# Kernel tuning notes

Hardware: AMD Instinct MI355X
Metric: run time of the kernel (lower is better)

## Reference

```python
import jax, jax.numpy as jnp
import numpy as np

EPS = 1e-5

def bn_eval(x, p):
    # p: [4, C] = gamma, beta, running_mean, running_var; channel-last broadcast
    g, b, m, v = p[0], p[1], p[2], p[3]
    return (x - m) * (g / jnp.sqrt(v + EPS)) + b

def _bn_params(k, c):
    k1, k2, k3, k4 = jax.random.split(k, 4)
    gamma = jax.random.uniform(k1, (c,)) + 0.5
    beta = jax.random.normal(k2, (c,)) * 0.1
    mean = jax.random.normal(k3, (c,)) * 0.1
    var = jax.random.uniform(k4, (c,)) + 0.5
    return jnp.stack([gamma, beta, mean, var])

def _lin(k, fan_in, fan_out):
    bound = 1.0 / np.sqrt(fan_in)
    kw, kb = jax.random.split(k)
    w = jax.random.uniform(kw, (fan_in, fan_out), minval=-bound, maxval=bound)
    b = jax.random.uniform(kb, (fan_out,), minval=-bound, maxval=bound)
    return w, b

def setup_inputs() -> dict:
    key = jax.random.key(0)
    B, N, S, C, G = 2, 4096, 16, 256, 8
    ks = jax.random.split(key, 20)
    feats = jax.random.normal(ks[0], (B, N, C), dtype=jnp.float32)
    coords = jax.random.normal(ks[1], (B, N, 3), dtype=jnp.float32)
    index = jax.random.randint(ks[2], (B, N, S), 0, N, dtype=jnp.int32)
    wq, bq = _lin(ks[3], C, C); bnq = _bn_params(ks[4], C)
    wk, bk = _lin(ks[5], C, C); bnk = _bn_params(ks[6], C)
    wv, bv = _lin(ks[7], C, C)
    pm_w1, pm_b1 = _lin(ks[8], 3, C); pm_bn = _bn_params(ks[9], C)
    pm_w2, pm_b2 = _lin(ks[10], C, C)
    pb_w1, pb_b1 = _lin(ks[11], 3, C); pb_bn = _bn_params(ks[12], C)
    pb_w2, pb_b2 = _lin(ks[13], C, C)
    we_w1, we_b1 = _lin(ks[14], C, G); we_bn = _bn_params(ks[15], G)
    we_w2, we_b2 = _lin(ks[16], G, G)
    return dict(feats=feats, coords=coords, index=index,
                wq=wq, bq=bq, bnq=bnq, wk=wk, bk=bk, bnk=bnk, wv=wv, bv=bv,
                pm_w1=pm_w1, pm_b1=pm_b1, pm_bn=pm_bn, pm_w2=pm_w2, pm_b2=pm_b2,
                pb_w1=pb_w1, pb_b1=pb_b1, pb_bn=pb_bn, pb_w2=pb_w2, pb_b2=pb_b2,
                we_w1=we_w1, we_b1=we_b1, we_bn=we_bn, we_w2=we_w2, we_b2=we_b2)

def reference(feats, coords, index,
              wq, bq, bnq, wk, bk, bnk, wv, bv,
              pm_w1, pm_b1, pm_bn, pm_w2, pm_b2,
              pb_w1, pb_b1, pb_bn, pb_w2, pb_b2,
              we_w1, we_b1, we_bn, we_w2, we_b2):
    B, N, C = feats.shape
    S = index.shape[2]
    G = we_w1.shape[1]
    q = jax.nn.relu(bn_eval(feats @ wq + bq, bnq))                       # [B,N,C]
    k = jax.nn.relu(bn_eval(feats @ wk + bk, bnk))                       # [B,N,C]
    v = feats @ wv + bv                                                   # [B,N,C]
    idx = index.reshape(B, N * S)
    key_g = jnp.take_along_axis(k, idx[:, :, None], axis=1).reshape(B, N, S, C)
    val_g = jnp.take_along_axis(v, idx[:, :, None], axis=1).reshape(B, N, S, C)
    crd_g = jnp.take_along_axis(coords, idx[:, :, None], axis=1).reshape(B, N, S, 3)
    relation_qk = key_g - q[:, :, None, :]                                # [B,N,S,C]
    pos = coords[:, :, None, :] - crd_g                                   # [B,N,S,3]
    pem = jax.nn.relu(bn_eval(pos @ pm_w1 + pm_b1, pm_bn)) @ pm_w2 + pm_b2
    relation_qk = relation_qk * pem
    peb = jax.nn.relu(bn_eval(pos @ pb_w1 + pb_b1, pb_bn)) @ pb_w2 + pb_b2
    relation_qk = relation_qk + peb
    val_g = val_g + peb
    w = jax.nn.relu(bn_eval(relation_qk @ we_w1 + we_b1, we_bn)) @ we_w2 + we_b2  # [B,N,S,G]
    w = jax.nn.softmax(w, axis=2)                                         # softmax over neighbors
    val_g = val_g.reshape(B, N, S, G, C // G)
    out = jnp.einsum('bnsgi,bnsg->bngi', val_g, w).reshape(B, N, C)
    return out
```

## Files before the change

kernel.cpp:

```cpp
#include <hip/hip_runtime.h>
#include <hip/hip_bf16.h>


typedef __attribute__((ext_vector_type(8))) short bf16x8_t;
typedef __attribute__((ext_vector_type(4))) float f32x4_t;

#define BN_EPS 1e-5f
#define WSYNC() asm volatile("s_waitcnt lgkmcnt(0)" ::: "memory")

__device__ __forceinline__ float blo(unsigned int v) {
    union { unsigned int u; float f; } x; x.u = v << 16; return x.f;
}
__device__ __forceinline__ float bhi(unsigned int v) {
    union { unsigned int u; float f; } x; x.u = v & 0xffff0000u; return x.f;
}
__device__ __forceinline__ unsigned int fbits(float f) {
    union { float f; unsigned int u; } x; x.f = f; return x.u;
}
__device__ __forceinline__ unsigned short f2b(float f) {
    unsigned int u = fbits(f);
    return (unsigned short)((u + 0x7fffu + ((u >> 16) & 1u)) >> 16);
}
__device__ __forceinline__ unsigned int f2bpk(float a, float b) {
    union { __hip_bfloat162 h; unsigned int u; } x;
    x.h = __float22bfloat162_rn(make_float2(a, b));
    return x.u;
}
__device__ __forceinline__ unsigned int relpair(unsigned int kb, unsigned int qb,
                                                unsigned int pm_, unsigned int pb_) {
    float r0 = (blo(kb) - blo(qb)) * blo(pm_) + blo(pb_);
    float r1 = (bhi(kb) - bhi(qb)) * bhi(pm_) + bhi(pb_);
    return f2bpk(r0, r1);
}

__global__ __launch_bounds__(256) void k_prep(
    const float* __restrict__ wq, const float* __restrict__ wk,
    const float* __restrict__ wv, const float* __restrict__ pm2,
    const float* __restrict__ pb2,
    const float* __restrict__ pm_w1, const float* __restrict__ pm_b1,
    const float* __restrict__ pm_bn,
    const float* __restrict__ pb_w1, const float* __restrict__ pb_b1,
    const float* __restrict__ pb_bn,
    const float* __restrict__ we_w1,
    unsigned short* __restrict__ wsT, float* __restrict__ W4,
    unsigned short* __restrict__ we1TF)
{
    const int bid = blockIdx.x, t = threadIdx.x;
    if (bid < 160) {
        __shared__ unsigned short T[32][72];
        const int mat = bid >> 5;
        const int kk  = (bid >> 2) & 7;
        const int ntq = bid & 3;
        const float* s = (mat == 0) ? wq : (mat == 1) ? wk : (mat == 2) ? wv
                         : (mat == 3) ? pm2 : pb2;
        {
            int c = t & 63, r0 = t >> 6;
            for (int i = 0; i < 8; ++i) {
                int r = r0 + i * 4;
                T[r][c] = f2b(s[(kk * 32 + r) * 256 + ntq * 64 + c]);
            }
        }
        __syncthreads();
        {
            int seg = t >> 6, lane = t & 63;
            int col = seg * 16 + (lane & 15);
            int kr  = (lane >> 4) * 8;
            unsigned int v[8];
            #pragma unroll
            for (int j = 0; j < 8; ++j) v[j] = T[kr + j][col];
            uint4 o;
            o.x = v[0] | (v[1] << 16);
            o.y = v[2] | (v[3] << 16);
            o.z = v[4] | (v[5] << 16);
            o.w = v[6] | (v[7] << 16);
            *(uint4*)(wsT + mat * 65536 + (ntq * 4 + seg) * 4096 + kk * 512 + lane * 8) = o;
        }
    } else if (bid == 160) {
        int c = t;
        float s = pm_bn[c] / sqrtf(pm_bn[768 + c] + BN_EPS);
        float4 wm = make_float4(pm_w1[c] * s, pm_w1[256 + c] * s, pm_w1[512 + c] * s,
                                (pm_b1[c] - pm_bn[512 + c]) * s + pm_bn[256 + c]);
        s = pb_bn[c] / sqrtf(pb_bn[768 + c] + BN_EPS);
        float4 wb = make_float4(pb_w1[c] * s, pb_w1[256 + c] * s, pb_w1[512 + c] * s,
                                (pb_b1[c] - pb_bn[512 + c]) * s + pb_bn[256 + c]);
        ((float4*)W4)[c]       = wm;
        ((float4*)W4)[256 + c] = wb;
    } else {
        for (int j = 0; j < 8; ++j) {
            int e = t * 8 + j;
            int g = e >> 8, c = e & 255;
            we1TF[g * 256 + c] = f2b(we_w1[c * 8 + g]);
        }
    }
}

__global__ __launch_bounds__(256) void k_qkv(
    const float* __restrict__ feats,
    const unsigned short* __restrict__ wT,
    const float* __restrict__ bq, const float* __restrict__ bnq,
    const float* __restrict__ bk, const float* __restrict__ bnk,
    const float* __restrict__ bv,
    unsigned short* __restrict__ qkv)
{
    __shared__ unsigned short A[32][264];
    const int t    = threadIdx.x;
    const int widx = blockIdx.x >> 8;
    const int mb   = blockIdx.x & 255;

    for (int i = 0; i < 8; ++i) {
        int row = 4 * i + (t >> 6), col = (t & 63) * 4;
        float4 f = *(const float4*)(feats + (mb * 32 + row) * 256 + col);
        *(uint2*)&A[row][col] = make_uint2(f2bpk(f.x, f.y), f2bpk(f.z, f.w));
    }
    __syncthreads();

    const int lane = t & 63, w = t >> 6;
    const int ln15 = lane & 15, quad = lane >> 4;
    const int mt = w & 1, nh = w >> 1;

    bf16x8_t afr[8];
    #pragma unroll
    for (int kk = 0; kk < 8; ++kk)
        afr[kk] = *(const bf16x8_t*)&A[mt * 16 + ln15][kk * 32 + quad * 8];

    const unsigned short* W = wT + widx * 65536;
    const float* bias = (widx == 0) ? bq : (widx == 1) ? bk : bv;
    const float* bn   = (widx == 0) ? bnq : (widx == 1) ? bnk : nullptr;
    unsigned short* dst = qkv + (size_t)widx * 8192 * 256;

    f32x4_t acc[8];
    for (int j = 0; j < 8; ++j) acc[j] = (f32x4_t){0.f, 0.f, 0.f, 0.f};

    #pragma unroll
    for (int kk = 0; kk < 8; ++kk) {
        #pragma unroll
        for (int j = 0; j < 8; ++j) {
            int nt = nh * 8 + j;
            bf16x8_t bfr = *(const bf16x8_t*)(W + ((nt * 8 + kk) * 64 + lane) * 8);
            acc[j] = __builtin_amdgcn_mfma_f32_16x16x32_bf16(afr[kk], bfr, acc[j], 0, 0, 0);
        }
    }

    float bb[8], sc[8], mu[8], be[8];
    #pragma unroll
    for (int j = 0; j < 8; ++j) {
        int c = (nh * 8 + j) * 16 + ln15;
        bb[j] = bias[c];
        if (bn) {
            sc[j] = bn[c] / sqrtf(bn[768 + c] + BN_EPS);
            be[j] = bn[256 + c];
            mu[j] = bn[512 + c];
        }
    }
    __syncthreads();
    #pragma unroll
    for (int j = 0; j < 8; ++j) {
        int c = (nh * 8 + j) * 16 + ln15;
        float y[4];
        for (int r = 0; r < 4; ++r) {
            y[r] = acc[j][r] + bb[j];
            if (bn) y[r] = fmaxf((y[r] - mu[j]) * sc[j] + be[j], 0.f);
        }
        for (int r = 0; r < 4; r += 2) {
            unsigned int pk = f2bpk(y[r], y[r + 1]);
            A[mt * 16 + quad * 4 + r][c]     = (unsigned short)pk;
            A[mt * 16 + quad * 4 + r + 1][c] = (unsigned short)(pk >> 16);
        }
    }
    __syncthreads();
    {
        int row = t >> 3, cc = (t & 7) * 32;
        #pragma unroll
        for (int j = 0; j < 4; ++j) {
            uint4 v = *(const uint4*)&A[row][cc + 8 * j];
            *(uint4*)(dst + (mb * 32 + row) * 256 + cc + 8 * j) = v;
        }
    }
}

__global__ __launch_bounds__(512, 4) void k_main(
    const float* __restrict__ coords,
    const int*   __restrict__ index,
    const unsigned short* __restrict__ qm,
    const unsigned short* __restrict__ km,
    const unsigned short* __restrict__ vm,
    const unsigned short* __restrict__ pmw2F,
    const unsigned short* __restrict__ pbw2F,
    const float* __restrict__ W4,
    const unsigned short* __restrict__ we1TF,
    const float* __restrict__ pm_b2, const float* __restrict__ pb_b2,
    const float* __restrict__ we_b1, const float* __restrict__ we_bn,
    const float* __restrict__ we_w2, const float* __restrict__ we_b2,
    float* __restrict__ out)
{
    __shared__ unsigned short bufR[64][264];
    __shared__ unsigned short bufP[64][264];
    __shared__ float posA[64][4];
    __shared__ float usP[2][64][8];
    __shared__ float us_[64][8];
    __shared__ int   rowg_[64];
    __shared__ float we2s[8][8];
    __shared__ float web2[8], swe8[8], dwe8[8];

    const int t   = threadIdx.x;
    const int P0  = blockIdx.x * 4;
    const int bb_ = P0 >> 12;
    const int w = t >> 6, lane = t & 63;
    const int ln15 = lane & 15, quad = lane >> 4;
    const int p   = w >> 1, sub = w & 1;
    const int R0  = p * 16;
    const int Pg  = P0 + p;

    const int rg = (bb_ << 12) + index[Pg * 16 + ln15];
    uint4 kpre[4];
    #pragma unroll
    for (int kk = 0; kk < 4; ++kk)
        kpre[kk] = *(const uint4*)(km + rg * 256 + (sub * 4 + kk) * 32 + quad * 8);

    if (lane < 8) {
        int m  = w * 8 + lane;
        int Pr = P0 + (m >> 4);
        int rs = (bb_ << 12) + index[Pr * 16 + (m & 15)];
        rowg_[m]   = rs;
        posA[m][0] = coords[Pr * 3 + 0] - coords[rs * 3 + 0];
        posA[m][1] = coords[Pr * 3 + 1] - coords[rs * 3 + 1];
        posA[m][2] = coords[Pr * 3 + 2] - coords[rs * 3 + 2];
        posA[m][3] = 0.f;
    }
    if (t < 64) we2s[t >> 3][t & 7] = we_w2[t];
    if (t < 8) {
        float s = we_bn[t] / sqrtf(we_bn[24 + t] + BN_EPS);
        swe8[t] = s;
        dwe8[t] = (we_b1[t] - we_bn[16 + t]) * s + we_bn[8 + t];
        web2[t] = we_b2[t];
    }
    WSYNC();

    const int hc = lane * 4;
    const int hm = w * 8;

    {
        float4 c0 = ((const float4*)W4)[256 + hc];
        float4 c1 = ((const float4*)W4)[256 + hc + 1];
        float4 c2 = ((const float4*)W4)[256 + hc + 2];
        float4 c3 = ((const float4*)W4)[256 + hc + 3];
        #pragma unroll
        for (int m = 0; m < 8; ++m) {
            float4 pp = *(const float4*)&posA[hm + m][0];
            float h0 = fmaxf(pp.x * c0.x + pp.y * c0.y + pp.z * c0.z + c0.w, 0.f);
            float h1 = fmaxf(pp.x * c1.x + pp.y * c1.y + pp.z * c1.z + c1.w, 0.f);
            float h2 = fmaxf(pp.x * c2.x + pp.y * c2.y + pp.z * c2.z + c2.w, 0.f);
            float h3 = fmaxf(pp.x * c3.x + pp.y * c3.y + pp.z * c3.z + c3.w, 0.f);
            *(uint2*)&bufR[hm + m][hc] = make_uint2(f2bpk(h0, h1), f2bpk(h2, h3));
        }
    }
    __syncthreads();

    f32x4_t acc[2][4];
    {
        float b0 = pb_b2[(w * 2    ) * 16 + ln15];
        float b1 = pb_b2[(w * 2 + 1) * 16 + ln15];
        for (int mt = 0; mt < 4; ++mt) {
            acc[0][mt] = (f32x4_t){b0, b0, b0, b0};
            acc[1][mt] = (f32x4_t){b1, b1, b1, b1};
        }
    }
    #pragma unroll
    for (int kk = 0; kk < 8; ++kk) {
        bf16x8_t afr[4];
        #pragma unroll
        for (int mt = 0; mt < 4; ++mt)
            afr[mt] = *(const bf16x8_t*)&bufR[mt * 16 + ln15][kk * 32 + quad * 8];
        #pragma unroll
        for (int ntl = 0; ntl < 2; ++ntl) {
            int nt = w * 2 + ntl;
            bf16x8_t bfr = *(const bf16x8_t*)(pbw2F + ((nt * 8 + kk) * 64 + lane) * 8);
            #pragma unroll
            for (int mt = 0; mt < 4; ++mt)
                acc[ntl][mt] = __builtin_amdgcn_mfma_f32_16x16x32_bf16(afr[mt], bfr, acc[ntl][mt], 0, 0, 0);
        }
    }
    __syncthreads();

    #pragma unroll
    for (int ntl = 0; ntl < 2; ++ntl) {
        int c = (w * 2 + ntl) * 16 + ln15;
        for (int mt = 0; mt < 4; ++mt)
            for (int r = 0; r < 4; r += 2) {
                unsigned int pk = f2bpk(acc[ntl][mt][r], acc[ntl][mt][r + 1]);
                bufP[mt * 16 + quad * 4 + r][c]     = (unsigned short)pk;
                bufP[mt * 16 + quad * 4 + r + 1][c] = (unsigned short)(pk >> 16);
            }
    }
    {
        float4 c0 = ((const float4*)W4)[hc];
        float4 c1 = ((const float4*)W4)[hc + 1];
        float4 c2 = ((const float4*)W4)[hc + 2];
        float4 c3 = ((const float4*)W4)[hc + 3];
        #pragma unroll
        for (int m = 0; m < 8; ++m) {
            float4 pp = *(const float4*)&posA[hm + m][0];
            float h0 = fmaxf(pp.x * c0.x + pp.y * c0.y + pp.z * c0.z + c0.w, 0.f);
            float h1 = fmaxf(pp.x * c1.x + pp.y * c1.y + pp.z * c1.z + c1.w, 0.f);
            float h2 = fmaxf(pp.x * c2.x + pp.y * c2.y + pp.z * c2.z + c2.w, 0.f);
            float h3 = fmaxf(pp.x * c3.x + pp.y * c3.y + pp.z * c3.z + c3.w, 0.f);
            *(uint2*)&bufR[hm + m][hc] = make_uint2(f2bpk(h0, h1), f2bpk(h2, h3));
        }
    }
    __syncthreads();

    {
        float b0 = pm_b2[(w * 2    ) * 16 + ln15];
        float b1 = pm_b2[(w * 2 + 1) * 16 + ln15];
        for (int mt = 0; mt < 4; ++mt) {
            acc[0][mt] = (f32x4_t){b0, b0, b0, b0};
            acc[1][mt] = (f32x4_t){b1, b1, b1, b1};
        }
    }
    #pragma unroll
    for (int kk = 0; kk < 8; ++kk) {
        bf16x8_t afr[4];
        #pragma unroll
        for (int mt = 0; mt < 4; ++mt)
            afr[mt] = *(const bf16x8_t*)&bufR[mt * 16 + ln15][kk * 32 + quad * 8];
        #pragma unroll
        for (int ntl = 0; ntl < 2; ++ntl) {
            int nt = w * 2 + ntl;
            bf16x8_t bfr = *(const bf16x8_t*)(pmw2F + ((nt * 8 + kk) * 64 + lane) * 8);
            #pragma unroll
            for (int mt = 0; mt < 4; ++mt)
                acc[ntl][mt] = __builtin_amdgcn_mfma_f32_16x16x32_bf16(afr[mt], bfr, acc[ntl][mt], 0, 0, 0);
        }
    }
    __syncthreads();

    #pragma unroll
    for (int ntl = 0; ntl < 2; ++ntl) {
        int c = (w * 2 + ntl) * 16 + ln15;
        for (int mt = 0; mt < 4; ++mt)
            for (int r = 0; r < 4; r += 2) {
                unsigned int pk = f2bpk(acc[ntl][mt][r], acc[ntl][mt][r + 1]);
                bufR[mt * 16 + quad * 4 + r][c]     = (unsigned short)pk;
                bufR[mt * 16 + quad * 4 + r + 1][c] = (unsigned short)(pk >> 16);
            }
    }
    __syncthreads();

    {
        const bf16x8_t bz = {0, 0, 0, 0, 0, 0, 0, 0};
        f32x4_t lacc = {0.f, 0.f, 0.f, 0.f};
        #pragma unroll
        for (int kk = 0; kk < 4; ++kk) {
            int cb8 = (sub * 4 + kk) * 32 + quad * 8;
            uint4 pm4 = *(const uint4*)&bufR[R0 + ln15][cb8];
            uint4 pb4 = *(const uint4*)&bufP[R0 + ln15][cb8];
            uint4 q4  = *(const uint4*)(qm + Pg * 256 + cb8);
            union { uint4 u; bf16x8_t v; } rr;
            rr.u.x = relpair(kpre[kk].x, q4.x, pm4.x, pb4.x);
            rr.u.y = relpair(kpre[kk].y, q4.y, pm4.y, pb4.y);
            rr.u.z = relpair(kpre[kk].z, q4.z, pm4.z, pb4.z);
            rr.u.w = relpair(kpre[kk].w, q4.w, pm4.w, pb4.w);
            bf16x8_t bfr = bz;
            if (ln15 < 8) bfr = *(const bf16x8_t*)(we1TF + ln15 * 256 + cb8);
            lacc = __builtin_amdgcn_mfma_f32_16x16x32_bf16(rr.v, bfr, lacc, 0, 0, 0);
        }
        if (ln15 < 8) {
            #pragma unroll
            for (int r = 0; r < 4; ++r)
                usP[sub][R0 + quad * 4 + r][ln15] = lacc[r];
        }
    }
    __syncthreads();

    if (sub == 0 && lane < 16) {
        int s = lane;
        float uv[8], l[8];
        #pragma unroll
        for (int g = 0; g < 8; ++g) {
            float x = usP[0][R0 + s][g] + usP[1][R0 + s][g];
            uv[g] = fmaxf(x * swe8[g] + dwe8[g], 0.f);
        }
        #pragma unroll
        for (int g = 0; g < 8; ++g) {
            float x = web2[g];
            for (int gp = 0; gp < 8; ++gp) x += uv[gp] * we2s[gp][g];
            l[g] = x;
        }
        #pragma unroll
        for (int g = 0; g < 8; ++g) us_[R0 + s][g] = l[g];
    }
    WSYNC();

    if (sub == 0 && lane < 8) {
        int g = lane;
        float mx = -1e30f;
        for (int s = 0; s < 16; ++s) mx = fmaxf(mx, us_[R0 + s][g]);
        float e[16], sum = 0.f;
        for (int s = 0; s < 16; ++s) { e[s] = __expf(us_[R0 + s][g] - mx); sum += e[s]; }
        float inv = 1.f / sum;
        for (int s = 0; s < 16; ++s) us_[R0 + s][g] = e[s] * inv;
    }
    __syncthreads();

    {
        int idx2 = sub * 64 + lane;
        int c5 = idx2 * 2, g = c5 >> 5;
        float a0 = 0.f, a1 = 0.f;
        #pragma unroll
        for (int s = 0; s < 16; ++s) {
            int rv = rowg_[R0 + s];
            float wv_ = us_[R0 + s][g];
            unsigned int v2 = *(const unsigned int*)(vm + rv * 256 + c5);
            unsigned int p2 = *(const unsigned int*)&bufP[R0 + s][c5];
            a0 += wv_ * (blo(v2) + blo(p2));
            a1 += wv_ * (bhi(v2) + bhi(p2));
        }
        *(float2*)(out + (size_t)Pg * 256 + c5) = make_float2(a0, a1);
    }
}

extern "C" void kernel_launch(void* const* d_in, const int* in_sizes, int n_in,
                              void* d_out, int out_size, void* d_ws, size_t ws_size,
                              hipStream_t stream)
{
    const float* feats  = (const float*)d_in[0];
    const float* coords = (const float*)d_in[1];
    const int*   index  = (const int*)d_in[2];
    const float* wq     = (const float*)d_in[3];
    const float* bq     = (const float*)d_in[4];
    const float* bnq    = (const float*)d_in[5];
    const float* wk     = (const float*)d_in[6];
    const float* bk     = (const float*)d_in[7];
    const float* bnk    = (const float*)d_in[8];
    const float* wv     = (const float*)d_in[9];
    const float* bv     = (const float*)d_in[10];
    const float* pm_w1  = (const float*)d_in[11];
    const float* pm_b1  = (const float*)d_in[12];
    const float* pm_bn  = (const float*)d_in[13];
    const float* pm_w2  = (const float*)d_in[14];
    const float* pm_b2  = (const float*)d_in[15];
    const float* pb_w1  = (const float*)d_in[16];
    const float* pb_b1  = (const float*)d_in[17];
    const float* pb_bn  = (const float*)d_in[18];
    const float* pb_w2  = (const float*)d_in[19];
    const float* pb_b2  = (const float*)d_in[20];
    const float* we_w1  = (const float*)d_in[21];
    const float* we_b1  = (const float*)d_in[22];
    const float* we_bn  = (const float*)d_in[23];
    const float* we_w2  = (const float*)d_in[24];
    const float* we_b2  = (const float*)d_in[25];

    unsigned short* qkv   = (unsigned short*)d_ws;
    unsigned short* wsT   = qkv + (size_t)3 * 8192 * 256;
    float*          W4    = (float*)(wsT + 5 * 65536);
    unsigned short* we1TF = (unsigned short*)(W4 + 2048);

    const size_t need = (size_t)13238272 + 8192 + 4096;
    if (ws_size < need) {
        hipMemsetAsync(d_out, 0, (size_t)out_size * 4, stream);
        return;
    }

    k_prep<<<162,  256, 0, stream>>>(wq, wk, wv, pm_w2, pb_w2,
                                     pm_w1, pm_b1, pm_bn,
                                     pb_w1, pb_b1, pb_bn,
                                     we_w1, wsT, W4, we1TF);
    k_qkv <<<768,  256, 0, stream>>>(feats, wsT, bq, bnq, bk, bnk, bv, qkv);
    k_main<<<2048, 512, 0, stream>>>(coords, index,
                                     qkv,
                                     qkv + (size_t)8192 * 256,
                                     qkv + (size_t)2 * 8192 * 256,
                                     wsT + 3 * 65536,
                                     wsT + 4 * 65536,
                                     W4, we1TF,
                                     pm_b2, pb_b2,
                                     we_b1, we_bn, we_w2, we_b2,
                                     (float*)d_out);
}
```

Before: 198.3 us.

## Compute positional first layers with split-bf16 MFMA instead of scalar FMAs

The 3->256 positional-encoding first layers (pm and pb) move from per-thread scalar FMA loops to MFMA. Inputs and weights are split into hi/lo bf16 pairs so the products keep near-fp32 accuracy, and the bias enters through a constant-one column. It also computes the pm hidden layer early so one barrier can be dropped, and prefetches q into registers before the relation stage. The cost is extra prep work, more LDS for the packed position matrix, and MFMA instructions on mostly zero-padded K.

Measured after the change: 198.1 us. About the same (-0.1%).

```diff
diff --git a/kernel.cpp b/kernel.cpp
--- a/kernel.cpp
+++ b/kernel.cpp
@@ -20,6 +20,9 @@
 __device__ __forceinline__ unsigned short f2b(float f) {
     unsigned int u = fbits(f);
     return (unsigned short)((u + 0x7fffu + ((u >> 16) & 1u)) >> 16);
+}
+__device__ __forceinline__ float b2f(unsigned short h) {
+    union { unsigned int u; float f; } x; x.u = ((unsigned int)h) << 16; return x.f;
 }
 __device__ __forceinline__ unsigned int f2bpk(float a, float b) {
     union { __hip_bfloat162 h; unsigned int u; } x;
@@ -42,7 +45,7 @@
     const float* __restrict__ pb_w1, const float* __restrict__ pb_b1,
     const float* __restrict__ pb_bn,
     const float* __restrict__ we_w1,
-    unsigned short* __restrict__ wsT, float* __restrict__ W4,
+    unsigned short* __restrict__ wsT, unsigned short* __restrict__ w1F,
     unsigned short* __restrict__ we1TF)
 {
     const int bid = blockIdx.x, t = threadIdx.x;
@@ -77,14 +80,28 @@
         }
     } else if (bid == 160) {
         int c = t;
-        float s = pm_bn[c] / sqrtf(pm_bn[768 + c] + BN_EPS);
-        float4 wm = make_float4(pm_w1[c] * s, pm_w1[256 + c] * s, pm_w1[512 + c] * s,
-                                (pm_b1[c] - pm_bn[512 + c]) * s + pm_bn[256 + c]);
-        s = pb_bn[c] / sqrtf(pb_bn[768 + c] + BN_EPS);
-        float4 wb = make_float4(pb_w1[c] * s, pb_w1[256 + c] * s, pb_w1[512 + c] * s,
-                                (pb_b1[c] - pb_bn[512 + c]) * s + pb_bn[256 + c]);
-        ((float4*)W4)[c]       = wm;
-        ((float4*)W4)[256 + c] = wb;
+        int nt = c >> 4, l15 = c & 15;
+        float sm = pm_bn[c] / sqrtf(pm_bn[768 + c] + BN_EPS);
+        float sb = pb_bn[c] / sqrtf(pb_bn[768 + c] + BN_EPS);
+        float W[2][4];
+        W[0][0] = pm_w1[c] * sm; W[0][1] = pm_w1[256 + c] * sm;
+        W[0][2] = pm_w1[512 + c] * sm;
+        W[0][3] = (pm_b1[c] - pm_bn[512 + c]) * sm + pm_bn[256 + c];
+        W[1][0] = pb_w1[c] * sb; W[1][1] = pb_w1[256 + c] * sb;
+        W[1][2] = pb_w1[512 + c] * sb;
+        W[1][3] = (pb_b1[c] - pb_bn[512 + c]) * sb + pb_bn[256 + c];
+        for (int pass = 0; pass < 2; ++pass) {
+            unsigned short xh = f2b(W[pass][0]), xl = f2b(W[pass][0] - b2f(xh));
+            unsigned short yh = f2b(W[pass][1]), yl = f2b(W[pass][1] - b2f(yh));
+            unsigned short zh = f2b(W[pass][2]), zl = f2b(W[pass][2] - b2f(zh));
+            unsigned short bh = f2b(W[pass][3]), bl = f2b(W[pass][3] - b2f(bh));
+            unsigned short sl[16] = { xh, xh, xl, yh, yh, yl, zh, zh, zl,
+                                      bh, bl, 0, 0, 0, 0, 0 };
+            for (int q = 0; q < 4; ++q)
+                for (int j = 0; j < 8; ++j)
+                    w1F[((pass * 16 + nt) * 64 + q * 16 + l15) * 8 + j] =
+                        (q < 2) ? sl[q * 8 + j] : (unsigned short)0;
+        }
     } else {
         for (int j = 0; j < 8; ++j) {
             int e = t * 8 + j;
@@ -186,7 +203,7 @@
     const unsigned short* __restrict__ vm,
     const unsigned short* __restrict__ pmw2F,
     const unsigned short* __restrict__ pbw2F,
-    const float* __restrict__ W4,
+    const unsigned short* __restrict__ w1F,
     const unsigned short* __restrict__ we1TF,
     const float* __restrict__ pm_b2, const float* __restrict__ pb_b2,
     const float* __restrict__ we_b1, const float* __restrict__ we_bn,
@@ -195,7 +212,7 @@
 {
     __shared__ unsigned short bufR[64][264];
     __shared__ unsigned short bufP[64][264];
-    __shared__ float posA[64][4];
+    __shared__ unsigned short posX[64][32];
     __shared__ float usP[2][64][8];
     __shared__ float us_[64][8];
     __shared__ int   rowg_[64];
@@ -217,45 +234,76 @@
     for (int kk = 0; kk < 4; ++kk)
         kpre[kk] = *(const uint4*)(km + rg * 256 + (sub * 4 + kk) * 32 + quad * 8);
 
-    if (lane < 8) {
-        int m  = w * 8 + lane;
+    if (t < 64) {
+        int m  = t;
         int Pr = P0 + (m >> 4);
         int rs = (bb_ << 12) + index[Pr * 16 + (m & 15)];
-        rowg_[m]   = rs;
-        posA[m][0] = coords[Pr * 3 + 0] - coords[rs * 3 + 0];
-        posA[m][1] = coords[Pr * 3 + 1] - coords[rs * 3 + 1];
-        posA[m][2] = coords[Pr * 3 + 2] - coords[rs * 3 + 2];
-        posA[m][3] = 0.f;
-    }
-    if (t < 64) we2s[t >> 3][t & 7] = we_w2[t];
+        rowg_[m] = rs;
+        float x = coords[Pr * 3 + 0] - coords[rs * 3 + 0];
+        float y = coords[Pr * 3 + 1] - coords[rs * 3 + 1];
+        float z = coords[Pr * 3 + 2] - coords[rs * 3 + 2];
+        unsigned short xh = f2b(x), xl = f2b(x - b2f(xh));
+        unsigned short yh = f2b(y), yl = f2b(y - b2f(yh));
+        unsigned short zh = f2b(z), zl = f2b(z - b2f(zh));
+        const unsigned short one = 0x3f80;
+        posX[m][0] = xh; posX[m][1] = xl; posX[m][2] = xh;
+        posX[m][3] = yh; posX[m][4] = yl; posX[m][5] = yh;
+        posX[m][6] = zh; posX[m][7] = zl; posX[m][8] = zh;
+        posX[m][9] = one; posX[m][10] = one;
+        #pragma unroll
+        for (int j2 = 11; j2 < 32; ++j2) posX[m][j2] = 0;
+        we2s[m >> 3][m & 7] = we_w2[m];
+    }
     if (t < 8) {
         float s = we_bn[t] / sqrtf(we_bn[24 + t] + BN_EPS);
         swe8[t] = s;
         dwe8[t] = (we_b1[t] - we_bn[16 + t]) * s + we_bn[8 + t];
         web2[t] = we_b2[t];
     }
-    WSYNC();
-
-    const int hc = lane * 4;
-    const int hm = w * 8;
+    __syncthreads();
+
+    bf16x8_t afrP[4];
+    #pragma unroll
+    for (int mt = 0; mt < 4; ++mt)
+        afrP[mt] = *(const bf16x8_t*)&posX[mt * 16 + ln15][quad * 8];
 
     {
-        float4 c0 = ((const float4*)W4)[256 + hc];
-        float4 c1 = ((const float4*)W4)[256 + hc + 1];
-        float4 c2 = ((const float4*)W4)[256 + hc + 2];
-        float4 c3 = ((const float4*)W4)[256 + hc + 3];
-        #pragma unroll
-        for (int m = 0; m < 8; ++m) {
-            float4 pp = *(const float4*)&posA[hm + m][0];
-            float h0 = fmaxf(pp.x * c0.x + pp.y * c0.y + pp.z * c0.z + c0.w, 0.f);
-            float h1 = fmaxf(pp.x * c1.x + pp.y * c1.y + pp.z * c1.z + c1.w, 0.f);
-            float h2 = fmaxf(pp.x * c2.x + pp.y * c2.y + pp.z * c2.z + c2.w, 0.f);
-            float h3 = fmaxf(pp.x * c3.x + pp.y * c3.y + pp.z * c3.z + c3.w, 0.f);
-            *(uint2*)&bufR[hm + m][hc] = make_uint2(f2bpk(h0, h1), f2bpk(h2, h3));
-        }
-    }
-    __syncthreads();
-
+        f32x4_t hb[2][4];
+        for (int ntl = 0; ntl < 2; ++ntl)
+            for (int mt = 0; mt < 4; ++mt) hb[ntl][mt] = (f32x4_t){0.f, 0.f, 0.f, 0.f};
+        #pragma unroll
+        for (int ntl = 0; ntl < 2; ++ntl) {
+            int nt = w * 2 + ntl;
+            bf16x8_t bfr = *(const bf16x8_t*)(w1F + ((16 + nt) * 64 + lane) * 8);
+            #pragma unroll
+            for (int mt = 0; mt < 4; ++mt)
+                hb[ntl][mt] = __builtin_amdgcn_mfma_f32_16x16x32_bf16(afrP[mt], bfr, hb[ntl][mt], 0, 0, 0);
+        }
+        #pragma unroll
+        for (int ntl = 0; ntl < 2; ++ntl) {
+            int c = (w * 2 + ntl) * 16 + ln15;
+            for (int mt = 0; mt < 4; ++mt)
+                for (int r = 0; r < 4; r += 2) {
+                    unsigned int pk = f2bpk(fmaxf(hb[ntl][mt][r], 0.f),
+                                            fmaxf(hb[ntl][mt][r + 1], 0.f));
+                    bufR[mt * 16 + quad * 4 + r][c]     = (unsigned short)pk;
+                    bufR[mt * 16 + quad * 4 + r + 1][c] = (unsigned short)(pk >> 16);
+                }
+        }
+    }
+    __syncthreads();
+
+    f32x4_t accM[2][4];
+    for (int ntl = 0; ntl < 2; ++ntl)
+        for (int mt = 0; mt < 4; ++mt) accM[ntl][mt] = (f32x4_t){0.f, 0.f, 0.f, 0.f};
+    #pragma unroll
+    for (int ntl = 0; ntl < 2; ++ntl) {
+        int nt = w * 2 + ntl;
+        bf16x8_t bfr = *(const bf16x8_t*)(w1F + (nt * 64 + lane) * 8);
+        #pragma unroll
+        for (int mt = 0; mt < 4; ++mt)
+            accM[ntl][mt] = __builtin_amdgcn_mfma_f32_16x16x32_bf16(afrP[mt], bfr, accM[ntl][mt], 0, 0, 0);
+    }
     f32x4_t acc[2][4];
     {
         float b0 = pb_b2[(w * 2    ) * 16 + ln15];
@@ -280,8 +328,6 @@
                 acc[ntl][mt] = __builtin_amdgcn_mfma_f32_16x16x32_bf16(afr[mt], bfr, acc[ntl][mt], 0, 0, 0);
         }
     }
-    __syncthreads();
-
     #pragma unroll
     for (int ntl = 0; ntl < 2; ++ntl) {
         int c = (w * 2 + ntl) * 16 + ln15;
@@ -292,23 +338,25 @@
                 bufP[mt * 16 + quad * 4 + r + 1][c] = (unsigned short)(pk >> 16);
             }
     }
-    {
-        float4 c0 = ((const float4*)W4)[hc];
-        float4 c1 = ((const float4*)W4)[hc + 1];
-        float4 c2 = ((const float4*)W4)[hc + 2];
-        float4 c3 = ((const float4*)W4)[hc + 3];
-        #pragma unroll
-        for (int m = 0; m < 8; ++m) {
-            float4 pp = *(const float4*)&posA[hm + m][0];
-            float h0 = fmaxf(pp.x * c0.x + pp.y * c0.y + pp.z * c0.z + c0.w, 0.f);
-            float h1 = fmaxf(pp.x * c1.x + pp.y * c1.y + pp.z * c1.z + c1.w, 0.f);
-            float h2 = fmaxf(pp.x * c2.x + pp.y * c2.y + pp.z * c2.z + c2.w, 0.f);
-            float h3 = fmaxf(pp.x * c3.x + pp.y * c3.y + pp.z * c3.z + c3.w, 0.f);
-            *(uint2*)&bufR[hm + m][hc] = make_uint2(f2bpk(h0, h1), f2bpk(h2, h3));
-        }
-    }
-    __syncthreads();
-
+    __syncthreads();
+
+    #pragma unroll
+    for (int ntl = 0; ntl < 2; ++ntl) {
+        int c = (w * 2 + ntl) * 16 + ln15;
+        for (int mt = 0; mt < 4; ++mt)
+            for (int r = 0; r < 4; r += 2) {
+                unsigned int pk = f2bpk(fmaxf(accM[ntl][mt][r], 0.f),
+                                        fmaxf(accM[ntl][mt][r + 1], 0.f));
+                bufR[mt * 16 + quad * 4 + r][c]     = (unsigned short)pk;
+                bufR[mt * 16 + quad * 4 + r + 1][c] = (unsigned short)(pk >> 16);
+            }
+    }
+    __syncthreads();
+
+    uint4 qpre[4];
+    #pragma unroll
+    for (int kk = 0; kk < 4; ++kk)
+        qpre[kk] = *(const uint4*)(qm + Pg * 256 + (sub * 4 + kk) * 32 + quad * 8);
     {
         float b0 = pm_b2[(w * 2    ) * 16 + ln15];
         float b1 = pm_b2[(w * 2 + 1) * 16 + ln15];
@@ -354,7 +402,7 @@
             int cb8 = (sub * 4 + kk) * 32 + quad * 8;
             uint4 pm4 = *(const uint4*)&bufR[R0 + ln15][cb8];
             uint4 pb4 = *(const uint4*)&bufP[R0 + ln15][cb8];
-            uint4 q4  = *(const uint4*)(qm + Pg * 256 + cb8);
+            uint4 q4  = qpre[kk];
             union { uint4 u; bf16x8_t v; } rr;
             rr.u.x = relpair(kpre[kk].x, q4.x, pm4.x, pb4.x);
             rr.u.y = relpair(kpre[kk].y, q4.y, pm4.y, pb4.y);
@@ -452,10 +500,10 @@
 
     unsigned short* qkv   = (unsigned short*)d_ws;
     unsigned short* wsT   = qkv + (size_t)3 * 8192 * 256;
-    float*          W4    = (float*)(wsT + 5 * 65536);
-    unsigned short* we1TF = (unsigned short*)(W4 + 2048);
-
-    const size_t need = (size_t)13238272 + 8192 + 4096;
+    unsigned short* we1TF = wsT + 5 * 65536;
+    unsigned short* w1F   = we1TF + 2048;
+
+    const size_t need = (size_t)13275136;
     if (ws_size < need) {
         hipMemsetAsync(d_out, 0, (size_t)out_size * 4, stream);
         return;
@@ -464,7 +512,7 @@
     k_prep<<<162,  256, 0, stream>>>(wq, wk, wv, pm_w2, pb_w2,
                                      pm_w1, pm_b1, pm_bn,
                                      pb_w1, pb_b1, pb_bn,
-                                     we_w1, wsT, W4, we1TF);
+                                     we_w1, wsT, w1F, we1TF);
     k_qkv <<<768,  256, 0, stream>>>(feats, wsT, bq, bnq, bk, bnk, bv, qkv);
     k_main<<<2048, 512, 0, stream>>>(coords, index,
                                      qkv,
@@ -472,7 +520,7 @@
                                      qkv + (size_t)2 * 8192 * 256,
                                      wsT + 3 * 65536,
                                      wsT + 4 * 65536,
-                                     W4, we1TF,
+                                     w1F, we1TF,
                                      pm_b2, pb_b2,
                                      we_b1, we_bn, we_w2, we_b2,
                                      (float*)d_out);
```
